# Performance work log

Measured on AMD Instinct MI355X. Metric: run time of the kernel, lower is better.

The kernel has to match this reference:

```python
import jax, jax.numpy as jnp
import numpy as np

REG_LAMBDA = 1e-4
NEG_SLOPE = 0.2
EPS = 1e-12


def _aggregate(edge_row, edge_col, edge_val, user_emb, item_emb, W_gcn, b_gcn, W_bi, b_bi):
    num_users = user_emb.shape[0]
    N = num_users + item_emb.shape[0]
    ego = jnp.concatenate([user_emb, item_emb], axis=0)  # [N, D]
    all_embs = [ego]
    n_layers = W_gcn.shape[0]
    for l in range(n_layers):
        # sparse adjacency spmm: side = A @ ego
        side = jax.ops.segment_sum(edge_val[:, None] * ego[edge_col], edge_row, num_segments=N)
        sum_e = side @ W_gcn[l] + b_gcn[l]
        bi_e = (ego * side) @ W_bi[l] + b_bi[l]
        ego = jax.nn.leaky_relu(sum_e + bi_e, negative_slope=NEG_SLOPE)
        # mess_dropout disabled (eval-mode); L2-normalize rows
        norm = jnp.maximum(jnp.linalg.norm(ego, axis=1, keepdims=True), EPS)
        all_embs.append(ego / norm)
    final = jnp.concatenate(all_embs, axis=1)  # [N, (L+1)*D]
    return final[:num_users], final[num_users:]


def reference(user, positive, negative, edge_row, edge_col, edge_val,
              user_emb, item_emb, W_gcn, b_gcn, W_bi, b_bi):
    users_all, items_all = _aggregate(edge_row, edge_col, edge_val,
                                      user_emb, item_emb, W_gcn, b_gcn, W_bi, b_bi)
    u = users_all[user]
    p = items_all[positive]
    n = items_all[negative]
    pos_score = jnp.sum(u * p, axis=1)
    neg_score = jnp.sum(u * n, axis=1)
    # BPR: -mean(log sigmoid(pos - neg)) == mean(softplus(neg - pos))
    bpr_loss = jnp.mean(jax.nn.softplus(neg_score - pos_score))
    ego_pos = item_emb[positive]
    ego_neg = item_emb[negative]
    B = user.shape[0]
    reg_loss = REG_LAMBDA * 0.5 * (jnp.sum(ego_pos ** 2) + jnp.sum(ego_neg ** 2)) / B
    return jnp.stack([bpr_loss, reg_loss])


def setup_inputs() -> dict:
    key = jax.random.key(0)
    ks = jax.random.split(key, 12)
    U, I, D, L, NNZ, B = 50000, 100000, 128, 3, 4800000, 4096
    N = U + I
    xav = (6.0 / (D + D)) ** 0.5
    return {
        "user": jax.random.randint(ks[0], (B,), 0, U, dtype=jnp.int32),
        "positive": jax.random.randint(ks[1], (B,), 0, I, dtype=jnp.int32),
        "negative": jax.random.randint(ks[2], (B,), 0, I, dtype=jnp.int32),
        "edge_row": jax.random.randint(ks[3], (NNZ,), 0, N, dtype=jnp.int32),
        "edge_col": jax.random.randint(ks[4], (NNZ,), 0, N, dtype=jnp.int32),
        "edge_val": jax.random.uniform(ks[5], (NNZ,), dtype=jnp.float32) / 32.0,
        "user_emb": jax.random.normal(ks[6], (U, D), dtype=jnp.float32) * 0.1,
        "item_emb": jax.random.normal(ks[7], (I, D), dtype=jnp.float32) * 0.1,
        "W_gcn": jax.random.uniform(ks[8], (L, D, D), minval=-xav, maxval=xav, dtype=jnp.float32),
        "b_gcn": jax.random.uniform(ks[9], (L, D), minval=-xav, maxval=xav, dtype=jnp.float32),
        "W_bi": jax.random.uniform(ks[10], (L, D, D), minval=-xav, maxval=xav, dtype=jnp.float32),
        "b_bi": jax.random.uniform(ks[11], (L, D), minval=-xav, maxval=xav, dtype=jnp.float32),
    }
```

## Files before the change

### kernel.cpp

```cpp
#include <hip/hip_runtime.h>
#include <math.h>

#define D 128
#define NEG_SLOPE 0.2f
#define REG_LAMBDA 1e-4f
#define NORM_EPS 1e-12f

#define RPB 256
#define RPB_SHIFT 8
#define MAXB 1024
#define CHUNK 4096
#define TCSH 14
#define KEYMAX 4096

#define XPAD 264

using bf16x8 = __attribute__((ext_vector_type(8))) short;
using f32x4  = __attribute__((ext_vector_type(4))) float;
using f32x2  = __attribute__((ext_vector_type(2))) float;

__device__ __forceinline__ float wave_red(float v){
  #pragma unroll
  for (int o = 32; o > 0; o >>= 1) v += __shfl_xor(v, o, 64);
  return v;
}

__device__ __forceinline__ unsigned short f2bf(float f){
  unsigned int u = __float_as_uint(f);
  unsigned int r = (u + 0x7fffu + ((u >> 16) & 1u)) >> 16;
  return (unsigned short)r;
}
__device__ __forceinline__ float bf_lo(unsigned int x){ return __uint_as_float(x << 16); }
__device__ __forceinline__ float bf_hi(unsigned int x){ return __uint_as_float(x & 0xffff0000u); }

__device__ __forceinline__ f32x2 pk_fma(f32x2 a, f32x2 b, f32x2 c){
  f32x2 d;
  asm("v_pk_fma_f32 %0, %1, %2, %3" : "=v"(d) : "v"(a), "v"(b), "v"(c));
  return d;
}
__device__ __forceinline__ unsigned int pk_bf16(float lo, float hi){
  unsigned int d;
  asm("v_cvt_pk_bf16_f32 %0, %1, %2" : "=v"(d) : "v"(lo), "v"(hi));
  return d;
}

__global__ __launch_bounds__(256) void toq_kernel(const float* __restrict__ src, unsigned int* __restrict__ dstb,
                                                  unsigned short* __restrict__ dst8, int npairs){
  int i = blockIdx.x*256 + threadIdx.x;
  if (i >= npairs) return;
  float2 v = ((const float2*)src)[i];
  dstb[i] = (unsigned int)f2bf(v.x) | ((unsigned int)f2bf(v.y) << 16);
  int p = __builtin_amdgcn_cvt_pk_fp8_f32(v.x, v.y, 0, false);
  dst8[i] = (unsigned short)(p & 0xffff);
}

__global__ __launch_bounds__(256) void wconv_kernel(const float* __restrict__ Wg, const float* __restrict__ Wb,
                                                    unsigned short* __restrict__ Wf, int L){
  int idx = blockIdx.x*256 + threadIdx.x;
  int total = L * 256 * D;
  if (idx >= total) return;
  int l = idx >> 15;
  int rem = idx & 32767;
  int k = rem >> 7;
  int n = rem & 127;
  float v = (k < 128) ? Wg[((size_t)l*128 + k)*D + n] : Wb[((size_t)l*128 + (k-128))*D + n];
  int ks = k >> 5, quad = (k >> 3) & 3, j = k & 7;
  int t = n >> 4, ln = (quad << 4) | (n & 15);
  Wf[(size_t)l*32768 + (((ks*8 + t)*64 + ln)*8 + j)] = f2bf(v);
}

__global__ __launch_bounds__(256) void bhist_kernel(const int* __restrict__ erow, int* __restrict__ bcnt, int nnz, int nbk){
  __shared__ int h[MAXB];
  for (int i = threadIdx.x; i < nbk; i += 256) h[i] = 0;
  __syncthreads();
  int stride = gridDim.x * 256;
  for (int e = blockIdx.x*256 + threadIdx.x; e < nnz; e += stride)
    atomicAdd(&h[erow[e] >> RPB_SHIFT], 1);
  __syncthreads();
  for (int i = threadIdx.x; i < nbk; i += 256){
    int c = h[i];
    if (c) atomicAdd(&bcnt[i], c);
  }
}

__global__ __launch_bounds__(1024) void bscan_kernel(const int* __restrict__ bcnt, int* __restrict__ bbase,
                                                     int* __restrict__ bcur, int* __restrict__ rowptr,
                                                     int nbk, int nnz, int n){
  __shared__ int tmp[1024];
  int t = threadIdx.x;
  int v = (t < nbk) ? bcnt[t] : 0;
  tmp[t] = v; __syncthreads();
  #pragma unroll
  for (int off = 1; off < 1024; off <<= 1){
    int a = (t >= off) ? tmp[t-off] : 0; __syncthreads();
    tmp[t] += a; __syncthreads();
  }
  if (t < nbk){ int b = tmp[t] - v; bbase[t] = b; bcur[t] = b; }
  if (t == 0){ bbase[nbk] = nnz; rowptr[n] = nnz; }
}

__global__ __launch_bounds__(256) void bscatter_kernel(const int* __restrict__ erow, const int* __restrict__ ecol,
                                                       const float* __restrict__ eval, int* __restrict__ bcur,
                                                       int2* __restrict__ ebuf, int nnz, int nbk){
  __shared__ int2 ls[CHUNK];
  __shared__ int gdst[CHUNK];
  __shared__ int h[MAXB];
  __shared__ int hx[MAXB];
  __shared__ int tmp[256];
  int tid = threadIdx.x;
  int base = blockIdx.x * CHUNK;
  int cn = min(CHUNK, nnz - base);
  for (int i = tid; i < nbk; i += 256) h[i] = 0;
  __syncthreads();
  for (int i = tid; i < cn; i += 256)
    atomicAdd(&h[erow[base+i] >> RPB_SHIFT], 1);
  __syncthreads();
  int b0 = tid*4;
  int c0=0,c1=0,c2=0,c3=0;
  if (b0 < nbk){
    c0 = h[b0];
    if (b0+1 < nbk) c1 = h[b0+1];
    if (b0+2 < nbk) c2 = h[b0+2];
    if (b0+3 < nbk) c3 = h[b0+3];
  }
  int tsum = c0+c1+c2+c3;
  tmp[tid] = tsum; __syncthreads();
  #pragma unroll
  for (int off = 1; off < 256; off <<= 1){
    int a = (tid >= off) ? tmp[tid-off] : 0; __syncthreads();
    tmp[tid] += a; __syncthreads();
  }
  int tbase = tmp[tid] - tsum;
  if (b0 < nbk){
    hx[b0] = tbase;
    if (b0+1 < nbk) hx[b0+1] = tbase + c0;
    if (b0+2 < nbk) hx[b0+2] = tbase + c0 + c1;
    if (b0+3 < nbk) hx[b0+3] = tbase + c0 + c1 + c2;
  }
  __syncthreads();
  for (int i = tid; i < nbk; i += 256){
    int c = h[i];
    if (c > 0){
      int gb = atomicAdd(&bcur[i], c);
      h[i] = gb - hx[i];
    }
  }
  __syncthreads();
  for (int i = tid; i < cn; i += 256){
    int r = erow[base+i];
    int b = r >> RPB_SHIFT;
    int x = ecol[base+i] | ((r & (RPB-1)) << 20);
    int lpos = atomicAdd(&hx[b], 1);
    ls[lpos] = make_int2(x, __float_as_int(eval[base+i]));
    gdst[lpos] = h[b] + lpos;
  }
  __syncthreads();
  for (int i = tid; i < cn; i += 256)
    ebuf[gdst[i]] = ls[i];
}

__global__ __launch_bounds__(256) void fscatter_kernel(const int2* __restrict__ ebuf, const int* __restrict__ bbase,
                                                       int2* __restrict__ ep, int* __restrict__ rowptr,
                                                       int Tc, int n){
  __shared__ int h[KEYMAX];
  __shared__ int tsum[256];
  int b = blockIdx.x;
  int tid = threadIdx.x;
  int s = bbase[b], e = bbase[b+1];
  int row0 = b << RPB_SHIFT;
  int nk = 256 * Tc;
  for (int i = tid; i < nk; i += 256) h[i] = 0;
  __syncthreads();
  for (int i = s + tid; i < e; i += 256){
    int x = ebuf[i].x;
    int key = ((x >> 20) & 255) * Tc + ((x & 0xFFFFF) >> TCSH);
    atomicAdd(&h[key], 1);
  }
  __syncthreads();
  int my0 = tid * Tc;
  int run = 0;
  for (int j = 0; j < Tc; j++){
    int c = h[my0 + j]; h[my0 + j] = run; run += c;
  }
  tsum[tid] = run; __syncthreads();
  #pragma unroll
  for (int off = 1; off < 256; off <<= 1){
    int a = (tid >= off) ? tsum[tid-off] : 0; __syncthreads();
    tsum[tid] += a; __syncthreads();
  }
  int bt = tsum[tid] - run;
  for (int j = 0; j < Tc; j++) h[my0 + j] += bt;
  __syncthreads();
  if (row0 + tid < n) rowptr[row0 + tid] = s + h[my0];
  __syncthreads();
  for (int i = s + tid; i < e; i += 256){
    int2 E = ebuf[i];
    int x = E.x;
    int col = x & 0xFFFFF;
    int key = ((x >> 20) & 255) * Tc + (col >> TCSH);
    int p = atomicAdd(&h[key], 1);
    ep[s + p] = make_int2(col << 7, E.y);
  }
}

__global__ __launch_bounds__(256) void spmm_kernel(const int* __restrict__ rowptr, const int2* __restrict__ ep,
                                                   const unsigned char* __restrict__ egof8,
                                                   unsigned int* __restrict__ sideb, int n){
  int w = (blockIdx.x*256 + threadIdx.x) >> 6;
  int lane = threadIdx.x & 63;
  if (w >= n) return;
  int s = rowptr[w], e = rowptr[w+1];
  int sub  = lane >> 4;
  int half = lane & 15;
  int half8 = half << 3;

  f32x2 acc2[4];
  #pragma unroll
  for (int j = 0; j < 4; j++) acc2[j] = (f32x2){0.f, 0.f};

  int base = s;
  for (; base + 32 <= e; base += 32){
    int2 E[8]; uint2 X[8];
    #pragma unroll
    for (int k = 0; k < 8; k++) E[k] = ep[base + 4*k + sub];
    #pragma unroll
    for (int k = 0; k < 8; k++)
      X[k] = *(const uint2*)(egof8 + (size_t)(unsigned)(E[k].x | half8));
    #pragma unroll
    for (int k = 0; k < 8; k++){
      float v = __int_as_float(E[k].y);
      f32x2 vv = (f32x2){v, v};
      acc2[0] = pk_fma(vv, __builtin_amdgcn_cvt_pk_f32_fp8((int)X[k].x, false), acc2[0]);
      acc2[1] = pk_fma(vv, __builtin_amdgcn_cvt_pk_f32_fp8((int)X[k].x, true ), acc2[1]);
      acc2[2] = pk_fma(vv, __builtin_amdgcn_cvt_pk_f32_fp8((int)X[k].y, false), acc2[2]);
      acc2[3] = pk_fma(vv, __builtin_amdgcn_cvt_pk_f32_fp8((int)X[k].y, true ), acc2[3]);
    }
  }
  for (; base < e; base += 16){
    int2 E[4]; uint2 X[4];
    #pragma unroll
    for (int k = 0; k < 4; k++){
      int idx = base + 4*k + sub;
      idx = idx < e ? idx : e - 1;
      E[k] = ep[idx];
    }
    #pragma unroll
    for (int k = 0; k < 4; k++)
      X[k] = *(const uint2*)(egof8 + (size_t)(unsigned)(E[k].x | half8));
    #pragma unroll
    for (int k = 0; k < 4; k++){
      float v = (base + 4*k + sub < e) ? __int_as_float(E[k].y) : 0.f;
      f32x2 vv = (f32x2){v, v};
      acc2[0] = pk_fma(vv, __builtin_amdgcn_cvt_pk_f32_fp8((int)X[k].x, false), acc2[0]);
      acc2[1] = pk_fma(vv, __builtin_amdgcn_cvt_pk_f32_fp8((int)X[k].x, true ), acc2[1]);
      acc2[2] = pk_fma(vv, __builtin_amdgcn_cvt_pk_f32_fp8((int)X[k].y, false), acc2[2]);
      acc2[3] = pk_fma(vv, __builtin_amdgcn_cvt_pk_f32_fp8((int)X[k].y, true ), acc2[3]);
    }
  }
  #pragma unroll
  for (int j = 0; j < 4; j++){
    acc2[j][0] += __shfl_xor(acc2[j][0], 16, 64);
    acc2[j][1] += __shfl_xor(acc2[j][1], 16, 64);
    acc2[j][0] += __shfl_xor(acc2[j][0], 32, 64);
    acc2[j][1] += __shfl_xor(acc2[j][1], 32, 64);
  }
  if (lane < 16){
    unsigned int o0 = pk_bf16(acc2[0][0], acc2[0][1]);
    unsigned int o1 = pk_bf16(acc2[1][0], acc2[1][1]);
    unsigned int o2 = pk_bf16(acc2[2][0], acc2[2][1]);
    unsigned int o3 = pk_bf16(acc2[3][0], acc2[3][1]);
    *(uint4*)(sideb + (size_t)w*64 + half*4) = make_uint4(o0, o1, o2, o3);
  }
}

__global__ __launch_bounds__(256, 4) void transform_kernel(const unsigned int* __restrict__ sideb,
                                                           unsigned int* __restrict__ egob,
                                                           unsigned char* __restrict__ egof8,
                                                           const unsigned short* __restrict__ Wf,
                                                           const float* __restrict__ b1, const float* __restrict__ b2,
                                                           int n){
  __shared__ __align__(16) unsigned short X[64 * XPAD];
  int row0 = blockIdx.x * 64;
  int tid = threadIdx.x;
  for (int idx = tid; idx < 64*64; idx += 256){
    int r = idx >> 6, cp = idx & 63;
    int row = row0 + r;
    unsigned int sv = 0, pv = 0;
    if (row < n){
      unsigned int s2 = sideb[(size_t)row*64 + cp];
      unsigned int eb = egob[(size_t)row*64 + cp];
      sv = s2;
      pv = (unsigned int)f2bf(bf_lo(s2) * bf_lo(eb)) | ((unsigned int)f2bf(bf_hi(s2) * bf_hi(eb)) << 16);
    }
    *(unsigned int*)&X[r*XPAD + 2*cp]       = sv;
    *(unsigned int*)&X[r*XPAD + 128 + 2*cp] = pv;
  }
  __syncthreads();

  int wave = tid >> 6, lane = tid & 63;
  int wr0 = wave * 16;
  int m = lane & 15, quad = lane >> 4;

  f32x4 acc[8];
  #pragma unroll
  for (int t = 0; t < 8; t++) acc[t] = (f32x4){0.f, 0.f, 0.f, 0.f};

  const unsigned short* arow = &X[(wr0 + m)*XPAD + quad*8];
  #pragma unroll
  for (int ks = 0; ks < 8; ks++){
    bf16x8 a = *(const bf16x8*)(arow + ks*32);
    #pragma unroll
    for (int t = 0; t < 8; t++){
      bf16x8 b = *(const bf16x8*)&Wf[((ks*8 + t)*64 + lane)*8];
      acc[t] = __builtin_amdgcn_mfma_f32_16x16x32_bf16(a, b, acc[t], 0, 0, 0);
    }
  }

  unsigned short* ego16 = (unsigned short*)egob;
  #pragma unroll
  for (int t = 0; t < 8; t++){
    int col = t*16 + m;
    float bb = b1[col] + b2[col];
    #pragma unroll
    for (int r = 0; r < 4; r++){
      int row = row0 + wr0 + quad*4 + r;
      if (row < n){
        float v = acc[t][r] + bb;
        v = v > 0.f ? v : NEG_SLOPE*v;
        ego16[(size_t)row*D + col] = f2bf(v);
        egof8[(size_t)row*D + col] =
            (unsigned char)(__builtin_amdgcn_cvt_pk_fp8_f32(v, v, 0, false) & 0xff);
      }
    }
  }
}

__global__ __launch_bounds__(256) void score_kernel(const unsigned int* __restrict__ egob, const int* __restrict__ user,
                                                    const int* __restrict__ pos, const int* __restrict__ neg,
                                                    float* __restrict__ pacc, float* __restrict__ nacc,
                                                    int B, int U, int normalize){
  int w = (blockIdx.x*256 + threadIdx.x) >> 6;
  int lane = threadIdx.x & 63;
  if (w >= B) return;
  size_t ur = (size_t)user[w] * 64;
  size_t pr = ((size_t)U + pos[w]) * 64;
  size_t nr = ((size_t)U + neg[w]) * 64;
  unsigned int ub = egob[ur + lane], pb = egob[pr + lane], nb = egob[nr + lane];
  float ux = bf_lo(ub), uy = bf_hi(ub);
  float px = bf_lo(pb), py = bf_hi(pb);
  float nx = bf_lo(nb), ny = bf_hi(nb);
  float dup = ux*px + uy*py;
  float dun = ux*nx + uy*ny;
  float nu  = ux*ux + uy*uy;
  float np  = px*px + py*py;
  float nn  = nx*nx + ny*ny;
  dup = wave_red(dup); dun = wave_red(dun);
  nu = wave_red(nu); np = wave_red(np); nn = wave_red(nn);
  if (lane == 0){
    if (normalize){
      float inu = 1.f / fmaxf(sqrtf(nu), NORM_EPS);
      float inp = 1.f / fmaxf(sqrtf(np), NORM_EPS);
      float inn = 1.f / fmaxf(sqrtf(nn), NORM_EPS);
      pacc[w] += dup * inu * inp;
      nacc[w] += dun * inu * inn;
    } else {
      pacc[w] += dup;
      nacc[w] += dun;
    }
  }
}

__global__ __launch_bounds__(256) void reg_kernel(const float* __restrict__ item, const int* __restrict__ pos,
                                                  const int* __restrict__ neg, float* __restrict__ reg_out, int B){
  int w = (blockIdx.x*256 + threadIdx.x) >> 6;
  int lane = threadIdx.x & 63;
  if (w >= B) return;
  const float2* it = (const float2*)item;
  float2 pv = it[(size_t)pos[w]*64 + lane];
  float2 nv = it[(size_t)neg[w]*64 + lane];
  float v = pv.x*pv.x + pv.y*pv.y + nv.x*nv.x + nv.y*nv.y;
  v = wave_red(v);
  if (lane == 0) atomicAdd(reg_out, v);
}

__global__ __launch_bounds__(256) void final_kernel(const float* __restrict__ pacc, const float* __restrict__ nacc,
                                                    const float* __restrict__ reg_sum, float* __restrict__ out, int B){
  __shared__ float red[256];
  float s = 0.f;
  for (int i = threadIdx.x; i < B; i += 256){
    float x = nacc[i] - pacc[i];
    s += (x > 0.f) ? x + log1pf(expf(-x)) : log1pf(expf(x));
  }
  red[threadIdx.x] = s; __syncthreads();
  for (int o = 128; o > 0; o >>= 1){
    if (threadIdx.x < o) red[threadIdx.x] += red[threadIdx.x + o];
    __syncthreads();
  }
  if (threadIdx.x == 0){
    out[0] = red[0] / (float)B;
    out[1] = REG_LAMBDA * 0.5f * reg_sum[0] / (float)B;
  }
}

extern "C" void kernel_launch(void* const* d_in, const int* in_sizes, int n_in,
                              void* d_out, int out_size, void* d_ws, size_t ws_size,
                              hipStream_t stream) {
  const int*   user = (const int*)d_in[0];
  const int*   pos  = (const int*)d_in[1];
  const int*   neg  = (const int*)d_in[2];
  const int*   erow = (const int*)d_in[3];
  const int*   ecol = (const int*)d_in[4];
  const float* eval = (const float*)d_in[5];
  const float* uemb = (const float*)d_in[6];
  const float* iemb = (const float*)d_in[7];
  const float* Wg   = (const float*)d_in[8];
  const float* bg   = (const float*)d_in[9];
  const float* Wb   = (const float*)d_in[10];
  const float* bb   = (const float*)d_in[11];

  int B   = in_sizes[0];
  int NNZ = in_sizes[3];
  int U   = in_sizes[6] / D;
  int I   = in_sizes[7] / D;
  int N   = U + I;
  int L   = in_sizes[9] / D;
  int nbk = (N + RPB - 1) >> RPB_SHIFT;
  int Tc  = (N + (1 << TCSH) - 1) >> TCSH;

  char* wsp = (char*)d_ws;
  auto alloc = [&](size_t bytes) -> char* {
    char* p = wsp; wsp += (bytes + 255) & ~(size_t)255; return p;
  };
  size_t side_bytes = (size_t)N * D * 2;
  size_t ebuf_bytes = (size_t)NNZ * 8;
  unsigned int*  sideb  = (unsigned int*)alloc(side_bytes > ebuf_bytes ? side_bytes : ebuf_bytes);
  unsigned int*  egob   = (unsigned int*)alloc((size_t)N * D * 2);
  unsigned short* egof8 = (unsigned short*)alloc((size_t)N * D);
  int2*          ep     = (int2*) alloc((size_t)NNZ * 8);
  unsigned short* Wf    = (unsigned short*)alloc((size_t)L * 256 * D * 2);
  int*           rowptr = (int*)  alloc((size_t)(N + 1) * 4);
  int*           bcnt   = (int*)  alloc((size_t)MAXB * 4);
  int*           bbase  = (int*)  alloc((size_t)(MAXB + 1) * 4);
  int*           bcur   = (int*)  alloc((size_t)MAXB * 4);
  float*         pacc   = (float*)alloc((size_t)B * 4);
  float*         nacc   = (float*)alloc((size_t)B * 4);
  float*         regs   = (float*)alloc(256);
  int2*          ebuf   = (int2*)sideb;

  hipMemsetAsync(bcnt, 0, (size_t)nbk * 4, stream);
  hipMemsetAsync(pacc, 0, (size_t)B * 4, stream);
  hipMemsetAsync(nacc, 0, (size_t)B * 4, stream);
  hipMemsetAsync(regs, 0, 4, stream);

  toq_kernel<<<(U*64 + 255) / 256, 256, 0, stream>>>(uemb, egob, egof8, U*64);
  toq_kernel<<<(I*64 + 255) / 256, 256, 0, stream>>>(iemb, egob + (size_t)U*64, egof8 + (size_t)U*64, I*64);
  wconv_kernel<<<(L*256*D + 255) / 256, 256, 0, stream>>>(Wg, Wb, Wf, L);

  bhist_kernel<<<2048, 256, 0, stream>>>(erow, bcnt, NNZ, nbk);
  bscan_kernel<<<1, 1024, 0, stream>>>(bcnt, bbase, bcur, rowptr, nbk, NNZ, N);
  bscatter_kernel<<<(NNZ + CHUNK - 1) / CHUNK, 256, 0, stream>>>(erow, ecol, eval, bcur, ebuf, NNZ, nbk);
  fscatter_kernel<<<nbk, 256, 0, stream>>>(ebuf, bbase, ep, rowptr, Tc, N);

  score_kernel<<<(B + 3) / 4, 256, 0, stream>>>(egob, user, pos, neg, pacc, nacc, B, U, 0);

  for (int l = 0; l < L; l++){
    spmm_kernel<<<(N + 3) / 4, 256, 0, stream>>>(rowptr, ep, (const unsigned char*)egof8, sideb, N);
    transform_kernel<<<(N + 63) / 64, 256, 0, stream>>>(
        sideb, egob, (unsigned char*)egof8, Wf + (size_t)l * 256 * D,
        bg + (size_t)l * D, bb + (size_t)l * D, N);
    score_kernel<<<(B + 3) / 4, 256, 0, stream>>>(egob, user, pos, neg, pacc, nacc, B, U, 1);
  }

  reg_kernel<<<(B + 3) / 4, 256, 0, stream>>>(iemb, pos, neg, regs, B);
  final_kernel<<<1, 256, 0, stream>>>(pacc, nacc, regs, (float*)d_out, B);
}
```

Measured before the change: 908.2 us.

## Compute last GCN layer only for rows sampled by users, positives and negatives

For the final propagation layer, the SpMM and dense transform now run only over the 3*B rows that the BPR score reads, not all N nodes. This drops most of the last layer's gather and MFMA work. Each row lookup goes through a small per-block table of sampled row indices. Duplicate sampled rows update ego in place, so one block may read a row another block has already overwritten, which risks a race on the previous-layer embedding.

```diff
diff --git a/kernel.cpp b/kernel.cpp
--- a/kernel.cpp
+++ b/kernel.cpp
@@ -203,13 +203,11 @@
   }
 }
 
-__global__ __launch_bounds__(256) void spmm_kernel(const int* __restrict__ rowptr, const int2* __restrict__ ep,
-                                                   const unsigned char* __restrict__ egof8,
-                                                   unsigned int* __restrict__ sideb, int n){
-  int w = (blockIdx.x*256 + threadIdx.x) >> 6;
-  int lane = threadIdx.x & 63;
-  if (w >= n) return;
-  int s = rowptr[w], e = rowptr[w+1];
+__device__ __forceinline__ void spmm_row_body(int row, int lane,
+                                              const int* __restrict__ rowptr, const int2* __restrict__ ep,
+                                              const unsigned char* __restrict__ egof8,
+                                              unsigned int* __restrict__ sideb){
+  int s = rowptr[row], e = rowptr[row+1];
   int sub  = lane >> 4;
   int half = lane & 15;
   int half8 = half << 3;
@@ -269,8 +267,36 @@
     unsigned int o1 = pk_bf16(acc2[1][0], acc2[1][1]);
     unsigned int o2 = pk_bf16(acc2[2][0], acc2[2][1]);
     unsigned int o3 = pk_bf16(acc2[3][0], acc2[3][1]);
-    *(uint4*)(sideb + (size_t)w*64 + half*4) = make_uint4(o0, o1, o2, o3);
-  }
+    *(uint4*)(sideb + (size_t)row*64 + half*4) = make_uint4(o0, o1, o2, o3);
+  }
+}
+
+__global__ __launch_bounds__(256) void spmm_kernel(const int* __restrict__ rowptr, const int2* __restrict__ ep,
+                                                   const unsigned char* __restrict__ egof8,
+                                                   unsigned int* __restrict__ sideb, int n){
+  int w = (blockIdx.x*256 + threadIdx.x) >> 6;
+  int lane = threadIdx.x & 63;
+  if (w >= n) return;
+  spmm_row_body(w, lane, rowptr, ep, egof8, sideb);
+}
+
+__device__ __forceinline__ int samp_row(int slot, const int* __restrict__ user, const int* __restrict__ pos,
+                                        const int* __restrict__ neg, int B, int U){
+  if (slot < B)   return user[slot];
+  if (slot < 2*B) return U + pos[slot - B];
+  return U + neg[slot - 2*B];
+}
+
+__global__ __launch_bounds__(256) void spmm_samp_kernel(const int* __restrict__ rowptr, const int2* __restrict__ ep,
+                                                        const unsigned char* __restrict__ egof8,
+                                                        unsigned int* __restrict__ sideb,
+                                                        const int* __restrict__ user, const int* __restrict__ pos,
+                                                        const int* __restrict__ neg, int B, int U){
+  int w = (blockIdx.x*256 + threadIdx.x) >> 6;
+  int lane = threadIdx.x & 63;
+  if (w >= 3*B) return;
+  int row = samp_row(w, user, pos, neg, B, U);
+  spmm_row_body(row, lane, rowptr, ep, egof8, sideb);
 }
 
 __global__ __launch_bounds__(256, 4) void transform_kernel(const unsigned int* __restrict__ sideb,
@@ -330,6 +356,73 @@
         ego16[(size_t)row*D + col] = f2bf(v);
         egof8[(size_t)row*D + col] =
             (unsigned char)(__builtin_amdgcn_cvt_pk_fp8_f32(v, v, 0, false) & 0xff);
+      }
+    }
+  }
+}
+
+__global__ __launch_bounds__(256, 4) void transform_samp_kernel(const unsigned int* __restrict__ sideb,
+                                                                unsigned int* __restrict__ egob,
+                                                                const unsigned short* __restrict__ Wf,
+                                                                const float* __restrict__ b1, const float* __restrict__ b2,
+                                                                const int* __restrict__ user, const int* __restrict__ pos,
+                                                                const int* __restrict__ neg, int B, int U){
+  __shared__ __align__(16) unsigned short X[64 * XPAD];
+  __shared__ int rows_l[64];
+  int slot0 = blockIdx.x * 64;
+  int tid = threadIdx.x;
+  int total = 3*B;
+  if (tid < 64){
+    int slot = slot0 + tid;
+    rows_l[tid] = (slot < total) ? samp_row(slot, user, pos, neg, B, U) : -1;
+  }
+  __syncthreads();
+  for (int idx = tid; idx < 64*64; idx += 256){
+    int r = idx >> 6, cp = idx & 63;
+    int row = rows_l[r];
+    unsigned int sv = 0, pv = 0;
+    if (row >= 0){
+      unsigned int s2 = sideb[(size_t)row*64 + cp];
+      unsigned int eb = egob[(size_t)row*64 + cp];
+      sv = s2;
+      pv = (unsigned int)f2bf(bf_lo(s2) * bf_lo(eb)) | ((unsigned int)f2bf(bf_hi(s2) * bf_hi(eb)) << 16);
+    }
+    *(unsigned int*)&X[r*XPAD + 2*cp]       = sv;
+    *(unsigned int*)&X[r*XPAD + 128 + 2*cp] = pv;
+  }
+  __syncthreads();
+
+  int wave = tid >> 6, lane = tid & 63;
+  int wr0 = wave * 16;
+  int m = lane & 15, quad = lane >> 4;
+
+  f32x4 acc[8];
+  #pragma unroll
+  for (int t = 0; t < 8; t++) acc[t] = (f32x4){0.f, 0.f, 0.f, 0.f};
+
+  const unsigned short* arow = &X[(wr0 + m)*XPAD + quad*8];
+  #pragma unroll
+  for (int ks = 0; ks < 8; ks++){
+    bf16x8 a = *(const bf16x8*)(arow + ks*32);
+    #pragma unroll
+    for (int t = 0; t < 8; t++){
+      bf16x8 b = *(const bf16x8*)&Wf[((ks*8 + t)*64 + lane)*8];
+      acc[t] = __builtin_amdgcn_mfma_f32_16x16x32_bf16(a, b, acc[t], 0, 0, 0);
+    }
+  }
+
+  unsigned short* ego16 = (unsigned short*)egob;
+  #pragma unroll
+  for (int t = 0; t < 8; t++){
+    int col = t*16 + m;
+    float bb = b1[col] + b2[col];
+    #pragma unroll
+    for (int r = 0; r < 4; r++){
+      int row = rows_l[wr0 + quad*4 + r];
+      if (row >= 0){
+        float v = acc[t][r] + bb;
+        v = v > 0.f ? v : NEG_SLOPE*v;
+        ego16[(size_t)row*D + col] = f2bf(v);
       }
     }
   }
@@ -463,11 +556,22 @@
 
   score_kernel<<<(B + 3) / 4, 256, 0, stream>>>(egob, user, pos, neg, pacc, nacc, B, U, 0);
 
+  int sampledN = 3 * B;
+  bool use_samp = (sampledN < N);
+
   for (int l = 0; l < L; l++){
-    spmm_kernel<<<(N + 3) / 4, 256, 0, stream>>>(rowptr, ep, (const unsigned char*)egof8, sideb, N);
-    transform_kernel<<<(N + 63) / 64, 256, 0, stream>>>(
-        sideb, egob, (unsigned char*)egof8, Wf + (size_t)l * 256 * D,
-        bg + (size_t)l * D, bb + (size_t)l * D, N);
+    if (use_samp && l == L - 1){
+      spmm_samp_kernel<<<(sampledN + 3) / 4, 256, 0, stream>>>(
+          rowptr, ep, (const unsigned char*)egof8, sideb, user, pos, neg, B, U);
+      transform_samp_kernel<<<(sampledN + 63) / 64, 256, 0, stream>>>(
+          sideb, egob, Wf + (size_t)l * 256 * D,
+          bg + (size_t)l * D, bb + (size_t)l * D, user, pos, neg, B, U);
+    } else {
+      spmm_kernel<<<(N + 3) / 4, 256, 0, stream>>>(rowptr, ep, (const unsigned char*)egof8, sideb, N);
+      transform_kernel<<<(N + 63) / 64, 256, 0, stream>>>(
+          sideb, egob, (unsigned char*)egof8, Wf + (size_t)l * 256 * D,
+          bg + (size_t)l * D, bb + (size_t)l * D, N);
+    }
     score_kernel<<<(B + 3) / 4, 256, 0, stream>>>(egob, user, pos, neg, pacc, nacc, B, U, 1);
   }
 
```

After: 799.7 us. 11.9% less time.
